# Performance work log

Measured on AMD Instinct MI355X. Metric: run time of the kernel, lower is better.

## Reference

```python
import jax, jax.numpy as jnp
import numpy as np

D = 4       # number of TT dimensions
N = 128     # mode size per dimension (Ns)
R = 16      # TT rank (RMAX)
B = 262144  # batch of query points


def setup_inputs() -> dict:
    key = jax.random.key(0)
    ks = jax.random.split(key, 5)
    # points in [-1, 1] (remap_needed=True assumes this domain)
    x = jax.random.uniform(ks[0], (B, D), dtype=jnp.float32) * 2.0 - 1.0
    core0 = jax.random.normal(ks[1], (1, N, R), dtype=jnp.float32)
    core1 = jax.random.normal(ks[2], (R, N, R), dtype=jnp.float32)
    core2 = jax.random.normal(ks[3], (R, N, R), dtype=jnp.float32)
    core3 = jax.random.normal(ks[4], (R, N, 1), dtype=jnp.float32)
    return {"x": x, "core0": core0, "core1": core1, "core2": core2, "core3": core3}


def _forward(x, cores):
    # remap: (x + 1) / 2 * (Ns[0] - 1)  (module uses Ns[0] for all dims)
    n0 = cores[0].shape[1]
    xr = (x + 1.0) * 0.5 * (n0 - 1)
    # per-dim clamp to [0, Ns[i]-1]
    ns = jnp.array([c.shape[1] for c in cores], dtype=x.dtype)  # [D]
    xc = jnp.clip(xr, 0.0, ns - 1.0)  # broadcast over D
    idx_low = jnp.floor(xc).astype(jnp.int32)   # [B, D]
    idx_high = jnp.ceil(xc).astype(jnp.int32)   # [B, D]
    wh = xc - idx_low.astype(x.dtype)           # [B, D] interpolation weights
    # gather + linear interpolation per core -> list of [r_prev, B, r_next]
    newcores = []
    for i, c in enumerate(cores):
        lo = jnp.take(c, idx_low[:, i], axis=1)   # [r_prev, B, r_next]
        hi = jnp.take(c, idx_high[:, i], axis=1)  # [r_prev, B, r_next]
        w = wh[:, i][None, :, None]               # [1, B, 1]
        newcores.append((1.0 - w) * lo + w * hi)
    # chained batched contraction, right to left (matches ttcontract)
    res = newcores[-1]
    for i in range(len(newcores) - 2, 0, -1):
        res = jnp.einsum('abc,cbk->abk', newcores[i], res)
    return jnp.einsum('abc,cbk->b', newcores[0], res)  # [B]


def reference(x, core0, core1, core2, core3):
    return _forward(x, [core0, core1, core2, core3])
```

## Files before the change

kernel.cpp:

```cpp
#include <hip/hip_runtime.h>
#include <hip/hip_bf16.h>

typedef unsigned int uint32;
typedef unsigned short u16;

#define NPT 128
#define RNK 16
#define MIDROW 264
#define MIDROW_U32 132
#define SMEM_BYTES (2*NPT*MIDROW*2)

#if defined(__has_builtin)
#if __has_builtin(__builtin_amdgcn_fdot2_f32_bf16)
#define HAVE_BFDOT2 1
#endif
#endif

__device__ __forceinline__ float bl(uint32 u){ return __uint_as_float(u << 16); }
__device__ __forceinline__ float bh(uint32 u){ return __uint_as_float(u & 0xffff0000u); }

__device__ __forceinline__ uint32 pk2(float a, float b){
  __hip_bfloat16 l = __float2bfloat16(a);
  __hip_bfloat16 h = __float2bfloat16(b);
  return (uint32)(*(u16*)&l) | ((uint32)(*(u16*)&h) << 16);
}

#ifdef HAVE_BFDOT2
typedef __bf16 v2bf __attribute__((ext_vector_type(2)));
__device__ __forceinline__ v2bf bc(uint32 u){ return __builtin_bit_cast(v2bf, u); }

__device__ __forceinline__ float dot16b(const uint32* vp, uint4 U0, uint4 U1) {
  float s0 = 0.f, s1 = 0.f;
  s0 = __builtin_amdgcn_fdot2_f32_bf16(bc(vp[0]), bc(U0.x), s0, false);
  s0 = __builtin_amdgcn_fdot2_f32_bf16(bc(vp[1]), bc(U0.y), s0, false);
  s0 = __builtin_amdgcn_fdot2_f32_bf16(bc(vp[2]), bc(U0.z), s0, false);
  s0 = __builtin_amdgcn_fdot2_f32_bf16(bc(vp[3]), bc(U0.w), s0, false);
  s1 = __builtin_amdgcn_fdot2_f32_bf16(bc(vp[4]), bc(U1.x), s1, false);
  s1 = __builtin_amdgcn_fdot2_f32_bf16(bc(vp[5]), bc(U1.y), s1, false);
  s1 = __builtin_amdgcn_fdot2_f32_bf16(bc(vp[6]), bc(U1.z), s1, false);
  s1 = __builtin_amdgcn_fdot2_f32_bf16(bc(vp[7]), bc(U1.w), s1, false);
  return s0 + s1;
}
#else
__device__ __forceinline__ float dot16(const float* v, uint4 U0, uint4 U1) {
  float s0 = fmaf(v[1],  bh(U0.x), v[0]*bl(U0.x));
  s0 = fmaf(v[2],  bl(U0.y), s0); s0 = fmaf(v[3],  bh(U0.y), s0);
  float s1 = fmaf(v[5],  bh(U0.z), v[4]*bl(U0.z));
  s1 = fmaf(v[6],  bl(U0.w), s1); s1 = fmaf(v[7],  bh(U0.w), s1);
  float s2 = fmaf(v[9],  bh(U1.x), v[8]*bl(U1.x));
  s2 = fmaf(v[10], bl(U1.y), s2); s2 = fmaf(v[11], bh(U1.y), s2);
  float s3 = fmaf(v[13], bh(U1.z), v[12]*bl(U1.z));
  s3 = fmaf(v[14], bl(U1.w), s3); s3 = fmaf(v[15], bh(U1.w), s3);
  return (s0 + s1) + (s2 + s3);
}
#endif

__device__ __forceinline__ float remap_clamp(float x) {
  float xr = (x + 1.0f) * 0.5f * (float)(NPT - 1);
  return fminf(fmaxf(xr, 0.0f), (float)(NPT - 1));
}

__device__ __forceinline__ void tt_mid(const uint32* __restrict__ base, float xc, float v[16]) {
  int n0 = min((int)xc, NPT - 2);
  float w = xc - (float)n0;
  const uint32* r0 = base + n0 * MIDROW_U32;
  const uint32* r1 = r0 + MIDROW_U32;

#ifdef HAVE_BFDOT2
  uint32 vp[8];
#pragma unroll
  for (int k = 0; k < 8; ++k) vp[k] = pk2(v[2*k], v[2*k+1]);
#endif

  float nv[16];
#pragma unroll
  for (int j = 0; j < 16; ++j) {
    const uint4* p0 = (const uint4*)(r0 + j * 8);
    const uint4* p1 = (const uint4*)(r1 + j * 8);
    uint4 A0 = p0[0], A1 = p0[1];
    uint4 B0 = p1[0], B1 = p1[1];
#ifdef HAVE_BFDOT2
    float a = dot16b(vp, A0, A1);
    float b = dot16b(vp, B0, B1);
#else
    float a = dot16(v, A0, A1);
    float b = dot16(v, B0, B1);
#endif
    nv[j] = fmaf(w, b - a, a);
  }
#pragma unroll
  for (int j = 0; j < 16; ++j) v[j] = nv[j];
}

__device__ __forceinline__ void stage_chunk(const float* __restrict__ g,
                                            u16* __restrict__ dst, int t) {
  int n = t >> 4, q = (t >> 1) & 7, h = t & 1;
  const float* s = g + (h * 8) * 2048 + n * 16 + q * 2;
  float2 f[8];
#pragma unroll
  for (int k = 0; k < 8; ++k) f[k] = *(const float2*)(s + k * 2048);
  uint4 w0, w1;
  w0.x = pk2(f[0].x, f[1].x); w0.y = pk2(f[2].x, f[3].x);
  w0.z = pk2(f[4].x, f[5].x); w0.w = pk2(f[6].x, f[7].x);
  w1.x = pk2(f[0].y, f[1].y); w1.y = pk2(f[2].y, f[3].y);
  w1.z = pk2(f[4].y, f[5].y); w1.w = pk2(f[6].y, f[7].y);
  *(uint4*)(dst + n * MIDROW + (2 * q) * 16 + h * 8)     = w0;
  *(uint4*)(dst + n * MIDROW + (2 * q + 1) * 16 + h * 8) = w1;
}

__global__ __launch_bounds__(1024, 1) void tt_kernel(
    const float* __restrict__ x,  const float* __restrict__ g0,
    const float* __restrict__ g1, const float* __restrict__ g2,
    const float* __restrict__ g3, float* __restrict__ out, int npts)
{
  extern __shared__ char smem[];
  u16* c1 = (u16*)smem;
  u16* c2 = c1 + NPT * MIDROW;

  const int tid = (int)threadIdx.x;
  const int p0i = (int)blockIdx.x * 1024 + tid;
  const int pc  = min(p0i, npts - 1);

  float4 xv = reinterpret_cast<const float4*>(x)[pc];

  stage_chunk(g1, c1, tid);
  stage_chunk(g1, c1, tid + 1024);
  stage_chunk(g2, c2, tid);
  stage_chunk(g2, c2, tid + 1024);

  float v[16];
  {
    float xc = remap_clamp(xv.x);
    int n0 = min((int)xc, NPT - 2);
    float w = xc - (float)n0;
    const float4* L = (const float4*)(g0 + n0 * 16);
#pragma unroll
    for (int k = 0; k < 4; ++k) {
      float4 l = L[k], h = L[k + 4];
      v[4*k+0] = fmaf(w, h.x - l.x, l.x);
      v[4*k+1] = fmaf(w, h.y - l.y, l.y);
      v[4*k+2] = fmaf(w, h.z - l.z, l.z);
      v[4*k+3] = fmaf(w, h.w - l.w, l.w);
    }
  }

  __syncthreads();

  tt_mid((const uint32*)c1, remap_clamp(xv.y), v);
  tt_mid((const uint32*)c2, remap_clamp(xv.z), v);

  float acc;
  {
    float xc = remap_clamp(xv.w);
    int n0 = min((int)xc, NPT - 2);
    float w = xc - (float)n0;
    float a0 = 0.f, a1 = 0.f, a2 = 0.f, a3 = 0.f;
#pragma unroll
    for (int i = 0; i < 4; ++i) {
#pragma unroll
      for (int k = 0; k < 4; ++k) {
        const float* col = g3 + (4 * i + k) * NPT + n0;
        float lo = col[0], hi = col[1];
        float cv = fmaf(w, hi - lo, lo);
        if (k == 0) a0 = fmaf(v[4*i+0], cv, a0);
        else if (k == 1) a1 = fmaf(v[4*i+1], cv, a1);
        else if (k == 2) a2 = fmaf(v[4*i+2], cv, a2);
        else a3 = fmaf(v[4*i+3], cv, a3);
      }
    }
    acc = (a0 + a1) + (a2 + a3);
  }
  if (p0i < npts) out[p0i] = acc;
}

extern "C" void kernel_launch(void* const* d_in, const int* in_sizes, int n_in,
                              void* d_out, int out_size, void* d_ws, size_t ws_size,
                              hipStream_t stream) {
  const float* x  = (const float*)d_in[0];
  const float* g0 = (const float*)d_in[1];
  const float* g1 = (const float*)d_in[2];
  const float* g2 = (const float*)d_in[3];
  const float* g3 = (const float*)d_in[4];
  float* out = (float*)d_out;

  int B = in_sizes[0] / 4;
  hipFuncSetAttribute(reinterpret_cast<const void*>(tt_kernel),
                      hipFuncAttributeMaxDynamicSharedMemorySize, SMEM_BYTES);
  int block = 1024;
  int grid = (B + block - 1) / block;
  tt_kernel<<<grid, block, SMEM_BYTES, stream>>>(x, g0, g1, g2, g3, out, B);
}
```

Measured before the change: 80.63 us.

## Stage mid cores with float4 loads and defer core2 smem write past core1 contraction

Staging now uses one float4-loading pass per thread per core instead of two float2 passes, with each thread writing four packed bf16 rows. Core2 is loaded into registers early, but its shared-memory write is delayed until after the core1 contraction and followed by a second barrier. The aim is wider global loads and hiding core2 staging latency behind core1 compute. The cost is more live registers (two 8x float4 arrays) and an extra __syncthreads.

```diff
diff --git a/kernel.cpp b/kernel.cpp
--- a/kernel.cpp
+++ b/kernel.cpp
@@ -92,20 +92,35 @@
   for (int j = 0; j < 16; ++j) v[j] = nv[j];
 }
 
-__device__ __forceinline__ void stage_chunk(const float* __restrict__ g,
-                                            u16* __restrict__ dst, int t) {
-  int n = t >> 4, q = (t >> 1) & 7, h = t & 1;
-  const float* s = g + (h * 8) * 2048 + n * 16 + q * 2;
-  float2 f[8];
-#pragma unroll
-  for (int k = 0; k < 8; ++k) f[k] = *(const float2*)(s + k * 2048);
-  uint4 w0, w1;
-  w0.x = pk2(f[0].x, f[1].x); w0.y = pk2(f[2].x, f[3].x);
-  w0.z = pk2(f[4].x, f[5].x); w0.w = pk2(f[6].x, f[7].x);
-  w1.x = pk2(f[0].y, f[1].y); w1.y = pk2(f[2].y, f[3].y);
-  w1.z = pk2(f[4].y, f[5].y); w1.w = pk2(f[6].y, f[7].y);
-  *(uint4*)(dst + n * MIDROW + (2 * q) * 16 + h * 8)     = w0;
-  *(uint4*)(dst + n * MIDROW + (2 * q + 1) * 16 + h * 8) = w1;
+__device__ __forceinline__ void stage_load4(const float* __restrict__ g, int t, float4* f) {
+  int n = t >> 3, jq = (t >> 1) & 3, h = t & 1;
+  const float* s = g + (h * 8) * 2048 + n * 16 + jq * 4;
+#pragma unroll
+  for (int k = 0; k < 8; ++k) f[k] = *(const float4*)(s + k * 2048);
+}
+__device__ __forceinline__ void stage_write4(u16* __restrict__ dst, int t, const float4* f) {
+  int n = t >> 3, jq = (t >> 1) & 3, h = t & 1;
+  u16* row = dst + n * MIDROW + h * 8;
+  {
+    uint4 w = make_uint4(pk2(f[0].x,f[1].x), pk2(f[2].x,f[3].x),
+                         pk2(f[4].x,f[5].x), pk2(f[6].x,f[7].x));
+    *(uint4*)(row + (4*jq+0) * 16) = w;
+  }
+  {
+    uint4 w = make_uint4(pk2(f[0].y,f[1].y), pk2(f[2].y,f[3].y),
+                         pk2(f[4].y,f[5].y), pk2(f[6].y,f[7].y));
+    *(uint4*)(row + (4*jq+1) * 16) = w;
+  }
+  {
+    uint4 w = make_uint4(pk2(f[0].z,f[1].z), pk2(f[2].z,f[3].z),
+                         pk2(f[4].z,f[5].z), pk2(f[6].z,f[7].z));
+    *(uint4*)(row + (4*jq+2) * 16) = w;
+  }
+  {
+    uint4 w = make_uint4(pk2(f[0].w,f[1].w), pk2(f[2].w,f[3].w),
+                         pk2(f[4].w,f[5].w), pk2(f[6].w,f[7].w));
+    *(uint4*)(row + (4*jq+3) * 16) = w;
+  }
 }
 
 __global__ __launch_bounds__(1024, 1) void tt_kernel(
@@ -122,31 +137,36 @@
   const int pc  = min(p0i, npts - 1);
 
   float4 xv = reinterpret_cast<const float4*>(x)[pc];
-
-  stage_chunk(g1, c1, tid);
-  stage_chunk(g1, c1, tid + 1024);
-  stage_chunk(g2, c2, tid);
-  stage_chunk(g2, c2, tid + 1024);
+  float xc0 = remap_clamp(xv.x);
+  int   d0n = min((int)xc0, NPT - 2);
+  float d0w = xc0 - (float)d0n;
+  const float4* Lg = (const float4*)(g0 + d0n * 16);
+
+  float4 f1[8];
+  stage_load4(g1, tid, f1);
+  stage_write4(c1, tid, f1);
+
+  float4 f2[8];
+  stage_load4(g2, tid, f2);
 
   float v[16];
-  {
-    float xc = remap_clamp(xv.x);
-    int n0 = min((int)xc, NPT - 2);
-    float w = xc - (float)n0;
-    const float4* L = (const float4*)(g0 + n0 * 16);
-#pragma unroll
-    for (int k = 0; k < 4; ++k) {
-      float4 l = L[k], h = L[k + 4];
-      v[4*k+0] = fmaf(w, h.x - l.x, l.x);
-      v[4*k+1] = fmaf(w, h.y - l.y, l.y);
-      v[4*k+2] = fmaf(w, h.z - l.z, l.z);
-      v[4*k+3] = fmaf(w, h.w - l.w, l.w);
-    }
+#pragma unroll
+  for (int k = 0; k < 4; ++k) {
+    float4 l = Lg[k], h = Lg[k + 4];
+    v[4*k+0] = fmaf(d0w, h.x - l.x, l.x);
+    v[4*k+1] = fmaf(d0w, h.y - l.y, l.y);
+    v[4*k+2] = fmaf(d0w, h.z - l.z, l.z);
+    v[4*k+3] = fmaf(d0w, h.w - l.w, l.w);
   }
 
   __syncthreads();
 
   tt_mid((const uint32*)c1, remap_clamp(xv.y), v);
+
+  stage_write4(c2, tid, f2);
+
+  __syncthreads();
+
   tt_mid((const uint32*)c2, remap_clamp(xv.z), v);
 
   float acc;
```

Result: slower. 135.2 us (+67.6%).

## Overlap core2 staging into shared memory with core1 contraction

Applied to the files above, without the earlier changes.

Core2's global loads, bf16 packing and shared-memory writes are moved to after the first barrier and interleaved with the core1 contraction, which runs in two halves. This lets core2's global load latency hide behind core1's dot-product compute instead of stalling before the first barrier. The cost is higher register pressure from holding the staged loads in flight, plus a second barrier that now separates the two stages.

```diff
diff --git a/kernel.cpp b/kernel.cpp
--- a/kernel.cpp
+++ b/kernel.cpp
@@ -60,6 +60,21 @@
   return fminf(fmaxf(xr, 0.0f), (float)(NPT - 1));
 }
 
+#ifdef HAVE_BFDOT2
+__device__ __forceinline__ void mid_slice(const uint32* r0, const uint32* r1, float w,
+                                          const uint32* vp, float* nv, int j0, int j1) {
+#pragma unroll
+  for (int j = j0; j < j1; ++j) {
+    const uint4* p0 = (const uint4*)(r0 + j * 8);
+    const uint4* p1 = (const uint4*)(r1 + j * 8);
+    uint4 A0 = p0[0], A1 = p0[1], B0 = p1[0], B1 = p1[1];
+    float a = dot16b(vp, A0, A1);
+    float b = dot16b(vp, B0, B1);
+    nv[j] = fmaf(w, b - a, a);
+  }
+}
+#endif
+
 __device__ __forceinline__ void tt_mid(const uint32* __restrict__ base, float xc, float v[16]) {
   int n0 = min((int)xc, NPT - 2);
   float w = xc - (float)n0;
@@ -70,35 +85,32 @@
   uint32 vp[8];
 #pragma unroll
   for (int k = 0; k < 8; ++k) vp[k] = pk2(v[2*k], v[2*k+1]);
-#endif
-
+  float nv[16];
+  mid_slice(r0, r1, w, vp, nv, 0, 16);
+#else
   float nv[16];
 #pragma unroll
   for (int j = 0; j < 16; ++j) {
     const uint4* p0 = (const uint4*)(r0 + j * 8);
     const uint4* p1 = (const uint4*)(r1 + j * 8);
-    uint4 A0 = p0[0], A1 = p0[1];
-    uint4 B0 = p1[0], B1 = p1[1];
-#ifdef HAVE_BFDOT2
-    float a = dot16b(vp, A0, A1);
-    float b = dot16b(vp, B0, B1);
-#else
+    uint4 A0 = p0[0], A1 = p0[1], B0 = p1[0], B1 = p1[1];
     float a = dot16(v, A0, A1);
     float b = dot16(v, B0, B1);
-#endif
     nv[j] = fmaf(w, b - a, a);
   }
+#endif
 #pragma unroll
   for (int j = 0; j < 16; ++j) v[j] = nv[j];
 }
 
-__device__ __forceinline__ void stage_chunk(const float* __restrict__ g,
-                                            u16* __restrict__ dst, int t) {
+__device__ __forceinline__ void stage_loads2(const float* __restrict__ g, int t, float2* f) {
   int n = t >> 4, q = (t >> 1) & 7, h = t & 1;
   const float* s = g + (h * 8) * 2048 + n * 16 + q * 2;
-  float2 f[8];
 #pragma unroll
   for (int k = 0; k < 8; ++k) f[k] = *(const float2*)(s + k * 2048);
+}
+__device__ __forceinline__ void stage_write2(u16* __restrict__ dst, int t, const float2* f) {
+  int n = t >> 4, q = (t >> 1) & 7, h = t & 1;
   uint4 w0, w1;
   w0.x = pk2(f[0].x, f[1].x); w0.y = pk2(f[2].x, f[3].x);
   w0.z = pk2(f[4].x, f[5].x); w0.w = pk2(f[6].x, f[7].x);
@@ -106,6 +118,12 @@
   w1.z = pk2(f[4].y, f[5].y); w1.w = pk2(f[6].y, f[7].y);
   *(uint4*)(dst + n * MIDROW + (2 * q) * 16 + h * 8)     = w0;
   *(uint4*)(dst + n * MIDROW + (2 * q + 1) * 16 + h * 8) = w1;
+}
+__device__ __forceinline__ void stage_chunk(const float* __restrict__ g,
+                                            u16* __restrict__ dst, int t) {
+  float2 f[8];
+  stage_loads2(g, t, f);
+  stage_write2(dst, t, f);
 }
 
 __global__ __launch_bounds__(1024, 1) void tt_kernel(
@@ -122,31 +140,63 @@
   const int pc  = min(p0i, npts - 1);
 
   float4 xv = reinterpret_cast<const float4*>(x)[pc];
+  float xc0 = remap_clamp(xv.x);
+  int   d0n = min((int)xc0, NPT - 2);
+  float d0w = xc0 - (float)d0n;
+  const float4* Lg = (const float4*)(g0 + d0n * 16);
 
   stage_chunk(g1, c1, tid);
   stage_chunk(g1, c1, tid + 1024);
-  stage_chunk(g2, c2, tid);
-  stage_chunk(g2, c2, tid + 1024);
 
   float v[16];
+#pragma unroll
+  for (int k = 0; k < 4; ++k) {
+    float4 l = Lg[k], h = Lg[k + 4];
+    v[4*k+0] = fmaf(d0w, h.x - l.x, l.x);
+    v[4*k+1] = fmaf(d0w, h.y - l.y, l.y);
+    v[4*k+2] = fmaf(d0w, h.z - l.z, l.z);
+    v[4*k+3] = fmaf(d0w, h.w - l.w, l.w);
+  }
+
+  __syncthreads();
+
   {
-    float xc = remap_clamp(xv.x);
+    float xc = remap_clamp(xv.y);
     int n0 = min((int)xc, NPT - 2);
     float w = xc - (float)n0;
-    const float4* L = (const float4*)(g0 + n0 * 16);
-#pragma unroll
-    for (int k = 0; k < 4; ++k) {
-      float4 l = L[k], h = L[k + 4];
-      v[4*k+0] = fmaf(w, h.x - l.x, l.x);
-      v[4*k+1] = fmaf(w, h.y - l.y, l.y);
-      v[4*k+2] = fmaf(w, h.z - l.z, l.z);
-      v[4*k+3] = fmaf(w, h.w - l.w, l.w);
-    }
+    const uint32* r0 = (const uint32*)c1 + n0 * MIDROW_U32;
+    const uint32* r1 = r0 + MIDROW_U32;
+
+#ifdef HAVE_BFDOT2
+    uint32 vp[8];
+#pragma unroll
+    for (int k = 0; k < 8; ++k) vp[k] = pk2(v[2*k], v[2*k+1]);
+
+    float2 fA[8];
+    stage_loads2(g2, tid, fA);
+
+    float nv[16];
+    mid_slice(r0, r1, w, vp, nv, 0, 8);
+
+    stage_write2(c2, tid, fA);
+    float2 fB[8];
+    stage_loads2(g2, tid + 1024, fB);
+
+    mid_slice(r0, r1, w, vp, nv, 8, 16);
+
+    stage_write2(c2, tid + 1024, fB);
+
+#pragma unroll
+    for (int j = 0; j < 16; ++j) v[j] = nv[j];
+#else
+    stage_chunk(g2, c2, tid);
+    stage_chunk(g2, c2, tid + 1024);
+    tt_mid((const uint32*)c1, xc, v);
+#endif
   }
 
   __syncthreads();
 
-  tt_mid((const uint32*)c1, remap_clamp(xv.y), v);
   tt_mid((const uint32*)c2, remap_clamp(xv.z), v);
 
   float acc;
```

New measurement: 124.6 us. 1.54x slower.
